# Performance work log

Measured on AMD Instinct MI355X. Metric: run time of the kernel, lower is better.

The kernel has to match this reference:

```python
import jax, jax.numpy as jnp
import numpy as np

B = 256          # graphs per batch
NN = 400         # ROI nodes per graph (N*(N-1)/2 = 79800 = input_dim)
HID = [32, 64, 128]
KS = [200, 100, 50]   # nodes kept after each TopKPooling (ratio 0.5 each)
EPS = 1e-5


def setup_inputs() -> dict:
    key = jax.random.key(0)
    ks = jax.random.split(key, 20)
    # flattened strict upper triangle of a nonnegative FC matrix per sample
    data = jax.random.uniform(ks[0], (B, NN * (NN - 1) // 2), dtype=jnp.float32)
    inp = {"data": data}
    dims = [1] + HID
    for l in range(3):
        fan_in = dims[l]
        inp[f"W{l+1}"] = jax.random.normal(ks[1 + 5 * l], (dims[l], dims[l + 1]), jnp.float32) / np.sqrt(fan_in)
        inp[f"b{l+1}"] = jnp.zeros((dims[l + 1],), jnp.float32)
        inp[f"g{l+1}"] = jnp.ones((dims[l + 1],), jnp.float32)      # BN gamma
        inp[f"be{l+1}"] = jnp.zeros((dims[l + 1],), jnp.float32)    # BN beta
        inp[f"p{l+1}"] = jax.random.normal(ks[4 + 5 * l], (dims[l + 1],), jnp.float32) * 0.1  # TopK score vector
    return inp


def _gcn_conv(A, X, W, b):
    # GCNConv with edge weights: add self loops (weight 1), symmetric D^-1/2 A D^-1/2
    n = A.shape[1]
    Al = A + jnp.eye(n, dtype=A.dtype)[None]          # (B, n, n)
    deg = Al.sum(axis=-1)                             # (B, n)
    dis = jnp.where(deg > 0, jax.lax.rsqrt(deg), 0.0)
    An = dis[:, :, None] * Al * dis[:, None, :]
    return jnp.einsum('bij,bjf->bif', An, X @ W) + b


def _block(A, X, W, b, g, be, p, k):
    # GCNConv -> ReLU -> BatchNorm(train stats) -> (dropout=identity) -> TopKPooling
    h = jax.nn.relu(_gcn_conv(A, X, W, b))
    mu = h.mean(axis=(0, 1))
    var = h.var(axis=(0, 1))
    h = (h - mu) * jax.lax.rsqrt(var + EPS) * g + be
    # TopKPooling: score = x . p / ||p||, keep top k per graph, gate by tanh(score)
    score = h @ p / jnp.linalg.norm(p)                # (B, n)
    vals, idx = jax.lax.top_k(score, k)               # (B, k)
    Xn = jnp.take_along_axis(h, idx[:, :, None], axis=1) * jnp.tanh(vals)[:, :, None]
    bi = jnp.arange(A.shape[0])[:, None, None]
    An = A[bi, idx[:, :, None], idx[:, None, :]]      # filter_adj: edges among kept nodes
    return An, Xn


def reference(data, W1, b1, g1, be1, p1, W2, b2, g2, be2, p2, W3, b3, g3, be3, p3):
    Bn = data.shape[0]
    iu0, iu1 = np.triu_indices(NN, 1)
    A = jnp.zeros((Bn, NN, NN), data.dtype).at[:, iu0, iu1].set(data)
    A = A + jnp.swapaxes(A, 1, 2)                     # symmetric FC adjacency, zero diag
    X = jnp.ones((Bn, NN, 1), data.dtype)             # initial node feature dim = 1
    A, X = _block(A, X, W1, b1, g1, be1, p1, KS[0])
    A, X = _block(A, X, W2, b2, g2, be2, p2, KS[1])
    A, X = _block(A, X, W3, b3, g3, be3, p3, KS[2])
    return X.max(axis=1)                              # global_max_pool -> (B, 128)
```

## Files before the change

kernel.cpp:

```cpp
#include <hip/hip_runtime.h>
#include <math.h>

#define BB   256
#define NN0  400
#define NE   79800
#define EPSF 1e-5f

__device__ __forceinline__ int tri_e(int a, int c) {
  return a*(NN0-1) - ((a*(a-1))>>1) + (c - a - 1);
}

__device__ __forceinline__ size_t PRI(int b, int ti, int tj, int r) {
  return (((size_t)b*7 + ti)*7 + tj)*64 + r;
}

__device__ __forceinline__ float wave_sum(float v) {
  #pragma unroll
  for (int o = 32; o > 0; o >>= 1) v += __shfl_xor(v, o, 64);
  return v;
}

__device__ __forceinline__ float rdlane(float v, int k) {
  return __int_as_float(__builtin_amdgcn_readlane(__float_as_int(v), k));
}

__device__ __forceinline__ void bitonic_desc(float* sc, int* si, int P) {
  const int tid = threadIdx.x;
  const int nt = blockDim.x;
  for (int k = 2; k <= P; k <<= 1) {
    for (int j = k >> 1; j > 0; j >>= 1) {
      __syncthreads();
      for (int i = tid; i < P; i += nt) {
        int ixj = i ^ j;
        if (ixj > i) {
          float a = sc[i], c = sc[ixj];
          int ai = si[i], ci = si[ixj];
          bool bef = (a > c) || (a == c && ai < ci);
          bool sw = ((i & k) == 0) ? !bef : bef;
          if (sw) { sc[i] = c; sc[ixj] = a; si[i] = ci; si[ixj] = ai; }
        }
      }
    }
  }
  __syncthreads();
}

__global__ __launch_bounds__(256) void k_tri_mv(
    const float* __restrict__ data,
    const float* __restrict__ pr_in, const float* __restrict__ pc_in,
    float* __restrict__ pr, float* __restrict__ pc) {
  __shared__ float tile[64][65];
  __shared__ float dI[64], dJ[64];
  const int xcd = blockIdx.x & 7, slot = blockIdx.x >> 3;
  const int b = xcd*32 + slot/7, q0 = slot % 7;
  const int tid = threadIdx.x;
  const int wave = tid >> 6, lane = tid & 63;
  const float* __restrict__ drow = data + (size_t)b*NE;
  int ti_a[4], tj_a[4];
  #pragma unroll
  for (int u = 0; u < 4; ++u) {
    int t = q0 + u*7;
    int ti = 0, rem = t;
    while (rem >= 7 - ti) { rem -= 7 - ti; ++ti; }
    ti_a[u] = ti; tj_a[u] = ti + rem;
  }
  float vreg[16];
  float rI = 0.f, rJ = 0.f;
  auto issue = [&](int u) {
    const int i0 = ti_a[u]*64, j0 = tj_a[u]*64;
    const int ni = min(64, NN0 - i0), nj = min(64, NN0 - j0);
    #pragma unroll
    for (int k = 0; k < 16; ++k) {
      const int rr = wave*16 + k;
      const int i = i0 + rr, j = j0 + lane;
      vreg[k] = 0.f;
      if (rr < ni && lane < nj && j > i) vreg[k] = drow[tri_e(i, j)];
    }
    if (pr_in) {
      if (tid < 64) {
        float a = 0.f;
        if (tid < ni) {
          const int tt = ti_a[u], r = tid;
          float acc = 1.f;
          for (int tj = tt; tj < 7; ++tj) acc += pr_in[PRI(b, tt, tj, r)];
          for (int ts = 0; ts <= tt; ++ts) acc += pc_in[PRI(b, ts, tt, r)];
          a = rsqrtf(acc);
        }
        rI = a;
      } else if (tid < 128) {
        const int c = tid - 64;
        float a = 0.f;
        if (c < nj) {
          const int tt = tj_a[u], r = c;
          float acc = 1.f;
          for (int tj = tt; tj < 7; ++tj) acc += pr_in[PRI(b, tt, tj, r)];
          for (int ts = 0; ts <= tt; ++ts) acc += pc_in[PRI(b, ts, tt, r)];
          a = rsqrtf(acc);
        }
        rJ = a;
      }
    } else {
      if (tid < 64) rI = (tid < ni) ? 1.f : 0.f;
      else if (tid < 128) rJ = (tid - 64 < nj) ? 1.f : 0.f;
    }
  };
  issue(0);
  #pragma unroll 1
  for (int u = 0; u < 4; ++u) {
    const int ti = ti_a[u], tj = tj_a[u];
    if (u) __syncthreads();
    #pragma unroll
    for (int k = 0; k < 16; ++k) tile[wave*16 + k][lane] = vreg[k];
    if (tid < 64) dI[tid] = rI;
    else if (tid < 128) dJ[tid-64] = rJ;
    __syncthreads();
    if (u + 1 < 4) issue(u + 1);
    {
      const int r = tid >> 2, q = tid & 3;
      float s = 0.f;
      #pragma unroll
      for (int c = 0; c < 16; ++c) s += tile[r][q*16 + c] * dJ[q*16 + c];
      s += __shfl_xor(s, 1, 64);
      s += __shfl_xor(s, 2, 64);
      if (q == 0) pr[PRI(b, ti, tj, r)] = s;
    }
    {
      const int c = tid >> 2, q = tid & 3;
      float s = 0.f;
      #pragma unroll
      for (int r = 0; r < 16; ++r) s += tile[q*16 + r][c] * dI[q*16 + r];
      s += __shfl_xor(s, 1, 64);
      s += __shfl_xor(s, 2, 64);
      if (q == 0) pc[PRI(b, ti, tj, c)] = s;
    }
  }
}

__global__ __launch_bounds__(256) void k_sfin_stats_red(
    const float* __restrict__ pr, const float* __restrict__ pc,
    const float* __restrict__ pr2, const float* __restrict__ pc2,
    const float* __restrict__ W1, const float* __restrict__ b1,
    float* __restrict__ s1, float* __restrict__ acc1) {
  __shared__ float sl[256];
  __shared__ float st[64];
  __shared__ float w1s[32], b1s[32];
  const int tid = threadIdx.x;
  const int i = blockIdx.x*256 + tid;
  if (tid < 32) { w1s[tid] = W1[tid]; b1s[tid] = b1[tid]; }
  if (tid < 64) st[tid] = 0.f;
  const int b = i / NN0, n = i % NN0;
  const int t = n >> 6, r = n & 63;
  float dacc = 1.f, sacc = 0.f;
  for (int tj = t; tj < 7; ++tj) { dacc += pr[PRI(b, t, tj, r)]; sacc += pr2[PRI(b, t, tj, r)]; }
  for (int ti = 0; ti <= t; ++ti) { dacc += pc[PRI(b, ti, t, r)]; sacc += pc2[PRI(b, ti, t, r)]; }
  const float d = rsqrtf(dacc);
  const float s = d * (d + sacc);
  s1[i] = s;
  sl[tid] = s;
  __syncthreads();
  const int f = tid & 31, sub = tid >> 5;
  const float w = w1s[f], bb = b1s[f];
  float S = 0.f, Q = 0.f;
  #pragma unroll
  for (int k = 0; k < 32; ++k) {
    const float ss = sl[sub*32 + k];
    const float h = fmaxf(ss*w + bb, 0.f);
    S += h; Q += h*h;
  }
  atomicAdd(&st[f], S);
  atomicAdd(&st[32+f], Q);
  __syncthreads();
  if (tid < 64) atomicAdd(&acc1[tid], st[tid]);
}

__global__ __launch_bounds__(512) void k_top1(
    const float* __restrict__ s1, const float* __restrict__ acc1,
    const float* __restrict__ W1, const float* __restrict__ b1,
    const float* __restrict__ g1, const float* __restrict__ be1,
    const float* __restrict__ p1, const float* __restrict__ W2,
    int* __restrict__ nodes2, int* __restrict__ sperm2, float* __restrict__ Y2) {
  __shared__ float sc[512]; __shared__ int si[512];
  __shared__ float sS[NN0];
  __shared__ float tvs[200];
  __shared__ int nds_l[200];
  __shared__ float w1s[32], b1s[32], cfs[32], scs[32], shs[32];
  __shared__ __align__(16) float hp[6400];
  __shared__ float c0s;
  const int tid = threadIdx.x;
  const int b = (blockIdx.x & 7)*32 + (blockIdx.x >> 3);
  if (tid < 32) { w1s[tid] = W1[tid]; b1s[tid] = b1[tid]; }
  if (tid < 64) {
    float scale = 0.f, shift = 0.f, pv = 0.f;
    if (tid < 32) {
      const float S = acc1[tid], Q = acc1[32 + tid];
      const float N = 102400.f;
      const float mu = S / N;
      const float var = Q / N - mu*mu;
      const float inv = rsqrtf(var + EPSF);
      scale = inv * g1[tid];
      shift = be1[tid] - mu * scale;
      pv = p1[tid];
    }
    const float pn = sqrtf(wave_sum(pv*pv));
    if (tid < 32) { scs[tid] = scale; shs[tid] = shift; cfs[tid] = scale*pv/pn; }
    float u = (tid < 32) ? shift*pv/pn : 0.f;
    u = wave_sum(u);
    if (tid == 0) c0s = u;
  }
  __syncthreads();
  const float c0 = c0s;
  {
    const int i = tid;
    if (i < NN0) {
      const float s = s1[(size_t)b*NN0 + i];
      sS[i] = s;
      float sco = c0;
      #pragma unroll
      for (int f = 0; f < 32; ++f) sco += fmaxf(s*w1s[f] + b1s[f], 0.f) * cfs[f];
      sc[i] = sco; si[i] = i;
    } else { sc[i] = -INFINITY; si[i] = 0x7fffffff; }
  }
  bitonic_desc(sc, si, 512);
  for (int k = tid; k < 200; k += 512) {
    tvs[k] = tanhf(sc[k]);
    nds_l[k] = si[k];
    nodes2[b*200 + k] = si[k];
  }
  __syncthreads();
  for (int o = tid; o < 6400; o += 512) {
    const int k = o >> 5, f = o & 31;
    const float s = sS[nds_l[k]];
    const float h = fmaxf(s*w1s[f] + b1s[f], 0.f);
    hp[o] = (h*scs[f] + shs[f]) * tvs[k];
  }
  __syncthreads();
  {
    const int g = tid & 63;
    float wr[32];
    #pragma unroll
    for (int f = 0; f < 32; ++f) wr[f] = W2[f*64 + g];
    for (int o = tid; o < 12800; o += 512) {
      const int k = o >> 6;
      float acc = 0.f;
      #pragma unroll
      for (int c4 = 0; c4 < 8; ++c4) {
        const float4 x4 = *(const float4*)&hp[(k<<5) + (c4<<2)];
        acc += x4.x*wr[c4*4] + x4.y*wr[c4*4+1] + x4.z*wr[c4*4+2] + x4.w*wr[c4*4+3];
      }
      Y2[(size_t)b*12800 + o] = acc;
    }
  }
  __syncthreads();
  if (tid < 256) {
    sc[tid] = (tid < 200) ? -(float)nds_l[tid] : -INFINITY;
    si[tid] = (tid < 200) ? tid : 0x7fffffff;
  }
  bitonic_desc(sc, si, 256);
  if (tid < 200) sperm2[b*200 + tid] = si[tid];
}

__global__ __launch_bounds__(256) void k_gatherA2(
    const float* __restrict__ data, const int* __restrict__ nodes2,
    const int* __restrict__ sperm2, float* __restrict__ A2, float* __restrict__ dis2) {
  __shared__ int nds[200], sp[200], sn[200];
  __shared__ float rowbuf[4][200];
  const int idx = blockIdx.x;
  const int r9 = idx >> 3;
  const int b = (idx & 7)*32 + r9/50;
  const int rg = r9 % 50;
  const int tid = threadIdx.x;
  if (tid < 200) { nds[tid] = nodes2[b*200 + tid]; sp[tid] = sperm2[b*200 + tid]; }
  __syncthreads();
  if (tid < 200) sn[tid] = nds[sp[tid]];
  __syncthreads();
  const int wave = tid >> 6, lane = tid & 63;
  const int i = rg*4 + wave;
  const int ni = nds[i];
  const float* __restrict__ drow = data + (size_t)b*NE;
  float accd = 0.f;
  for (int jj = lane; jj < 200; jj += 64) {
    const int sj = sn[jj];
    float v = 0.f;
    if (sj != ni) {
      const int a = min(ni, sj), c = max(ni, sj);
      v = drow[tri_e(a, c)];
    }
    rowbuf[wave][sp[jj]] = v;
    accd += v;
  }
  __syncthreads();
  accd = wave_sum(accd);
  const float dd = rsqrtf(1.f + accd);
  for (int j = lane; j < 200; j += 64)
    A2[((size_t)b*200 + i)*200 + j] = rowbuf[wave][j] * dd;
  if (lane == 0) dis2[b*200 + i] = dd;
}

__global__ __launch_bounds__(256) void k_conv2(
    const float* __restrict__ A2, const float* __restrict__ Y2,
    const float* __restrict__ dis2, const float* __restrict__ b2,
    float* __restrict__ h2g, float* __restrict__ acc2g) {
  __shared__ float dsb[200];
  __shared__ float st[128];
  const int tid = threadIdx.x;
  const int xcd = blockIdx.x & 7, slot = blockIdx.x >> 3;
  const int b = xcd*32 + (slot >> 3), p = slot & 7;
  const int wave = tid >> 6, lane = tid & 63;
  if (tid < 128) st[tid] = 0.f;
  if (tid < 200) dsb[tid] = dis2[b*200 + tid];
  __syncthreads();
  const float bl = b2[lane];
  const int rbl = p*25 + wave*7;
  const int lq = lane / 7, lk = lane - lq*7;
  const bool lv = (lane < 56) && (wave*7 + lk < 25);
  const float* __restrict__ Ab = A2 + (size_t)b*40000;
  const float* __restrict__ Yb = Y2 + (size_t)b*12800;
  auto ldA = [&](int j8) -> float {
    return lv ? Ab[(size_t)(j8 + lq)*200 + rbl + lk] : 0.f;
  };
  float acc[7];
  #pragma unroll
  for (int k = 0; k < 7; ++k) acc[k] = 0.f;
  float a_cur = ldA(0);
  #pragma unroll 1
  for (int jg = 0; jg < 25; ++jg) {
    const float a = a_cur;
    if (jg < 24) a_cur = ldA((jg + 1)*8);
    const int j0 = jg*8;
    #pragma unroll
    for (int q = 0; q < 8; ++q) {
      const float z = Yb[(j0 + q)*64 + lane];
      #pragma unroll
      for (int k = 0; k < 7; ++k)
        acc[k] = fmaf(rdlane(a, q*7 + k), z, acc[k]);
    }
  }
  float ss = 0.f, qq = 0.f;
  #pragma unroll
  for (int k = 0; k < 7; ++k) {
    const int lr = wave*7 + k;
    if (lr < 25) {
      const int r = p*25 + lr;
      const float d = dsb[r];
      const float y = Yb[(size_t)r*64 + lane];
      const float h = fmaxf(d*acc[k] + d*(d*y) + bl, 0.f);
      h2g[((size_t)b*200 + r)*64 + lane] = h;
      ss += h; qq += h*h;
    }
  }
  atomicAdd(&st[lane], ss);
  atomicAdd(&st[64 + lane], qq);
  __syncthreads();
  if (tid < 128) atomicAdd(&acc2g[tid], st[tid]);
}

__global__ __launch_bounds__(512) void k_top2(
    const float* __restrict__ h2g, const float* __restrict__ acc2,
    const float* __restrict__ g2, const float* __restrict__ be2,
    const float* __restrict__ p2, const float* __restrict__ W3,
    const int* __restrict__ nodes2, int* __restrict__ nodes3,
    float* __restrict__ Y3) {
  __shared__ float sc[256]; __shared__ int si[256];
  __shared__ __align__(16) float xs[6400];
  __shared__ float sc2[64], sh2[64], cf2[64];
  __shared__ float c20s;
  const int tid = threadIdx.x;
  const int b = (blockIdx.x & 7)*32 + (blockIdx.x >> 3);
  if (tid < 64) {
    const float S = acc2[tid], Q = acc2[64 + tid];
    const float N = 51200.f;
    const float mu = S/N, var = Q/N - mu*mu, inv = rsqrtf(var + EPSF);
    const float scale = inv*g2[tid], shift = be2[tid] - mu*scale;
    const float pv = p2[tid];
    const float pn = sqrtf(wave_sum(pv*pv));
    sc2[tid] = scale; sh2[tid] = shift; cf2[tid] = scale*pv/pn;
    const float u = wave_sum(shift*pv/pn);
    if (tid == 0) c20s = u;
  }
  __syncthreads();
  const int wave = tid >> 6, lane = tid & 63;
  const float cf = cf2[lane];
  const float c20 = c20s;
  for (int i = wave; i < 200; i += 8) {
    float v = h2g[((size_t)b*200 + i)*64 + lane] * cf;
    v = wave_sum(v);
    if (lane == 0) { sc[i] = v + c20; si[i] = i; }
  }
  if (tid >= 200 && tid < 256) { sc[tid] = -INFINITY; si[tid] = 0x7fffffff; }
  bitonic_desc(sc, si, 256);
  const float scale = sc2[lane], shift = sh2[lane];
  for (int o = tid; o < 6400; o += 512) {
    const int k = o >> 6;
    const int idx = si[k];
    const float tv = tanhf(sc[k]);
    xs[o] = (h2g[((size_t)b*200 + idx)*64 + lane] * scale + shift) * tv;
  }
  for (int k = tid; k < 100; k += 512) nodes3[b*100 + k] = nodes2[b*200 + si[k]];
  __syncthreads();
  {
    const int g = tid & 127;
    float wr[64];
    #pragma unroll
    for (int f = 0; f < 64; ++f) wr[f] = W3[f*128 + g];
    for (int o = tid; o < 12800; o += 512) {
      const int k = o >> 7;
      float acc = 0.f;
      #pragma unroll
      for (int c4 = 0; c4 < 16; ++c4) {
        const float4 x4 = *(const float4*)&xs[(k<<6) + (c4<<2)];
        acc += x4.x*wr[c4*4] + x4.y*wr[c4*4+1] + x4.z*wr[c4*4+2] + x4.w*wr[c4*4+3];
      }
      Y3[(size_t)b*12800 + o] = acc;
    }
  }
}

__global__ __launch_bounds__(256) void k_gatherA3(
    const float* __restrict__ data, const int* __restrict__ nodes3,
    float* __restrict__ A3, float* __restrict__ dis3) {
  __shared__ int nds[100];
  const int slot = blockIdx.x >> 3;
  const int b = (blockIdx.x & 7)*32 + slot/25, rg = slot % 25;
  const int tid = threadIdx.x;
  if (tid < 100) nds[tid] = nodes3[b*100 + tid];
  __syncthreads();
  const int wave = tid >> 6, lane = tid & 63;
  const int i = rg*4 + wave;
  const int ni = nds[i];
  const float* __restrict__ drow = data + (size_t)b*NE;
  const int j0 = lane, j1 = 64 + lane;
  float v0 = 0.f, v1 = 0.f;
  if (j0 != i) {
    const int nj = nds[j0];
    const int a = min(ni, nj), c = max(ni, nj);
    v0 = drow[tri_e(a, c)];
  }
  if (j1 < 100 && j1 != i) {
    const int nj = nds[j1];
    const int a = min(ni, nj), c = max(ni, nj);
    v1 = drow[tri_e(a, c)];
  }
  const float accd = wave_sum(v0 + v1);
  const float dd = rsqrtf(1.f + accd);
  A3[((size_t)b*100 + i)*100 + j0] = v0 * dd;
  if (j1 < 100) A3[((size_t)b*100 + i)*100 + j1] = v1 * dd;
  if (lane == 0) dis3[b*100 + i] = dd;
}

__global__ __launch_bounds__(256) void k_conv3(
    const float* __restrict__ A3, const float* __restrict__ Y3,
    const float* __restrict__ dis3, const float* __restrict__ b3,
    float* __restrict__ h3g, float* __restrict__ acc3g) {
  __shared__ float dsb[100];
  __shared__ float st[256];
  const int tid = threadIdx.x;
  const int xcd = blockIdx.x & 7, slot = blockIdx.x >> 3;
  const int b = xcd*32 + (slot >> 3), p = slot & 7;
  const int wave = tid >> 6, lane = tid & 63;
  st[tid] = 0.f;
  if (tid < 100) dsb[tid] = dis3[b*100 + tid];
  __syncthreads();
  const float bl0 = b3[lane], bl1 = b3[64 + lane];
  const int rbl = p*13 + wave*4;
  const int lq = lane >> 2, lk = lane & 3;
  const bool lvr = (wave*4 + lk < 13) && (rbl + lk < 100);
  const float* __restrict__ Ab = A3 + (size_t)b*10000;
  const float* __restrict__ Yb = Y3 + (size_t)b*12800;
  auto ldA = [&](int j16) -> float {
    return lvr ? Ab[(size_t)(j16 + lq)*100 + rbl + lk] : 0.f;
  };
  auto ldAt = [&](int j16) -> float {
    return (lvr && lq < 4) ? Ab[(size_t)(j16 + lq)*100 + rbl + lk] : 0.f;
  };
  float ac0[4], ac1[4];
  #pragma unroll
  for (int k = 0; k < 4; ++k) { ac0[k] = 0.f; ac1[k] = 0.f; }
  float a_cur = ldA(0);
  #pragma unroll 1
  for (int jg = 0; jg < 6; ++jg) {
    const float a = a_cur;
    a_cur = (jg < 5) ? ldA((jg + 1)*16) : ldAt(96);
    const int j0 = jg*16;
    #pragma unroll
    for (int q = 0; q < 16; ++q) {
      const float z0 = Yb[(j0 + q)*128 + lane];
      const float z1 = Yb[(j0 + q)*128 + 64 + lane];
      #pragma unroll
      for (int k = 0; k < 4; ++k) {
        const float av = rdlane(a, (q << 2) + k);
        ac0[k] = fmaf(av, z0, ac0[k]);
        ac1[k] = fmaf(av, z1, ac1[k]);
      }
    }
  }
  {
    const float a = a_cur;
    #pragma unroll
    for (int q = 0; q < 4; ++q) {
      const float z0 = Yb[(96 + q)*128 + lane];
      const float z1 = Yb[(96 + q)*128 + 64 + lane];
      #pragma unroll
      for (int k = 0; k < 4; ++k) {
        const float av = rdlane(a, (q << 2) + k);
        ac0[k] = fmaf(av, z0, ac0[k]);
        ac1[k] = fmaf(av, z1, ac1[k]);
      }
    }
  }
  float ss0 = 0.f, qq0 = 0.f, ss1 = 0.f, qq1 = 0.f;
  #pragma unroll
  for (int k = 0; k < 4; ++k) {
    const int lr = wave*4 + k;
    const int r = p*13 + lr;
    if (lr < 13 && r < 100) {
      const float d = dsb[r];
      const float y0 = Yb[(size_t)r*128 + lane];
      const float y1 = Yb[(size_t)r*128 + 64 + lane];
      const float h0 = fmaxf(d*ac0[k] + d*(d*y0) + bl0, 0.f);
      const float h1 = fmaxf(d*ac1[k] + d*(d*y1) + bl1, 0.f);
      h3g[((size_t)b*100 + r)*128 + lane] = h0;
      h3g[((size_t)b*100 + r)*128 + 64 + lane] = h1;
      ss0 += h0; qq0 += h0*h0; ss1 += h1; qq1 += h1*h1;
    }
  }
  atomicAdd(&st[lane], ss0);
  atomicAdd(&st[64 + lane], ss1);
  atomicAdd(&st[128 + lane], qq0);
  atomicAdd(&st[192 + lane], qq1);
  __syncthreads();
  atomicAdd(&acc3g[tid], st[tid]);
}

__global__ __launch_bounds__(256) void k_top3(
    const float* __restrict__ h3g, const float* __restrict__ acc3,
    const float* __restrict__ g3, const float* __restrict__ be3,
    const float* __restrict__ p3, float* __restrict__ out) {
  __shared__ float sc[128]; __shared__ int si[128]; __shared__ float tv[64];
  __shared__ float scl[128], shl[128], cfl[128];
  __shared__ float red2[4];
  const int tid = threadIdx.x;
  const int b = (blockIdx.x & 7)*32 + (blockIdx.x >> 3);
  const int wave = tid >> 6, lane = tid & 63;
  float scale = 0.f, shift = 0.f, pv = 0.f;
  if (tid < 128) {
    const float S = acc3[tid], Q = acc3[128 + tid];
    const float N = 25600.f;
    const float mu = S/N, var = Q/N - mu*mu, inv = rsqrtf(var + EPSF);
    scale = inv*g3[tid]; shift = be3[tid] - mu*scale; pv = p3[tid];
    const float t2 = wave_sum(pv*pv);
    if (lane == 0) red2[wave] = t2;
  }
  __syncthreads();
  const float pn = sqrtf(red2[0] + red2[1]);
  if (tid < 128) {
    scl[tid] = scale; shl[tid] = shift; cfl[tid] = scale*pv/pn;
    const float u = wave_sum(shift*pv/pn);
    if (lane == 0) red2[2 + wave] = u;
  }
  __syncthreads();
  const float c30 = red2[2] + red2[3];
  const float clo = cfl[lane], chi = cfl[64 + lane];
  for (int i = wave; i < 100; i += 4) {
    const float* hr = h3g + ((size_t)b*100 + i)*128;
    float v = hr[lane]*clo + hr[64 + lane]*chi;
    v = wave_sum(v);
    if (lane == 0) { sc[i] = v + c30; si[i] = i; }
  }
  if (tid >= 100 && tid < 128) { sc[tid] = -INFINITY; si[tid] = 0x7fffffff; }
  bitonic_desc(sc, si, 128);
  if (tid < 50) tv[tid] = tanhf(sc[tid]);
  __syncthreads();
  if (tid < 128) {
    const float scalev = scl[tid], shiftv = shl[tid];
    float m = -INFINITY;
    for (int k = 0; k < 50; ++k) {
      const float h = h3g[((size_t)b*100 + si[k])*128 + tid];
      m = fmaxf(m, (h*scalev + shiftv)*tv[k]);
    }
    out[(size_t)b*128 + tid] = m;
  }
}

extern "C" void kernel_launch(void* const* d_in, const int* in_sizes, int n_in,
                              void* d_out, int out_size, void* d_ws, size_t ws_size,
                              hipStream_t stream) {
  (void)in_sizes; (void)n_in; (void)out_size; (void)ws_size;
  const float* data = (const float*)d_in[0];
  const float* W1 = (const float*)d_in[1];
  const float* b1 = (const float*)d_in[2];
  const float* g1 = (const float*)d_in[3];
  const float* be1 = (const float*)d_in[4];
  const float* p1 = (const float*)d_in[5];
  const float* W2 = (const float*)d_in[6];
  const float* b2 = (const float*)d_in[7];
  const float* g2 = (const float*)d_in[8];
  const float* be2 = (const float*)d_in[9];
  const float* p2 = (const float*)d_in[10];
  const float* W3 = (const float*)d_in[11];
  const float* b3 = (const float*)d_in[12];
  const float* g3 = (const float*)d_in[13];
  const float* be3 = (const float*)d_in[14];
  const float* p3 = (const float*)d_in[15];
  float* out = (float*)d_out;

  char* ws = (char*)d_ws;
  size_t off = 0;
  auto alloc = [&](size_t n) { size_t o = off; off += (n + 255) & ~(size_t)255; return o; };
  float* pr     = (float*)(ws + alloc((size_t)BB*49*64*4));
  float* pc     = (float*)(ws + alloc((size_t)BB*49*64*4));
  float* pr2    = (float*)(ws + alloc((size_t)BB*49*64*4));
  float* pc2    = (float*)(ws + alloc((size_t)BB*49*64*4));
  float* s1     = (float*)(ws + alloc((size_t)BB*NN0*4));
  float* accz   = (float*)(ws + alloc(448*4));
  int*   nodes2 = (int*)  (ws + alloc((size_t)BB*200*4));
  int*   sperm2 = (int*)  (ws + alloc((size_t)BB*200*4));
  float* Y2     = (float*)(ws + alloc((size_t)BB*12800*4));
  float* A2     = (float*)(ws + alloc((size_t)BB*40000*4));
  float* dis2   = (float*)(ws + alloc((size_t)BB*200*4));
  float* h2     = (float*)(ws + alloc((size_t)BB*12800*4));
  int*   nodes3 = (int*)  (ws + alloc((size_t)BB*100*4));
  float* Y3     = (float*)(ws + alloc((size_t)BB*12800*4));
  float* A3     = (float*)(ws + alloc((size_t)BB*10000*4));
  float* dis3   = (float*)(ws + alloc((size_t)BB*100*4));
  float* h3     = (float*)(ws + alloc((size_t)BB*12800*4));
  float* acc1 = accz;
  float* acc2 = accz + 64;
  float* acc3 = accz + 192;

  hipMemsetAsync(accz, 0, 448*4, stream);
  k_tri_mv<<<dim3(BB*7), dim3(256), 0, stream>>>(data, nullptr, nullptr, pr, pc);
  k_tri_mv<<<dim3(BB*7), dim3(256), 0, stream>>>(data, pr, pc, pr2, pc2);
  k_sfin_stats_red<<<dim3(400), dim3(256), 0, stream>>>(pr, pc, pr2, pc2, W1, b1, s1, acc1);
  k_top1<<<dim3(BB), dim3(512), 0, stream>>>(s1, acc1, W1, b1, g1, be1, p1, W2, nodes2, sperm2, Y2);
  k_gatherA2<<<dim3(BB*50), dim3(256), 0, stream>>>(data, nodes2, sperm2, A2, dis2);
  k_conv2<<<dim3(BB*8), dim3(256), 0, stream>>>(A2, Y2, dis2, b2, h2, acc2);
  k_top2<<<dim3(BB), dim3(512), 0, stream>>>(h2, acc2, g2, be2, p2, W3, nodes2, nodes3, Y3);
  k_gatherA3<<<dim3(BB*25), dim3(256), 0, stream>>>(data, nodes3, A3, dis3);
  k_conv3<<<dim3(BB*8), dim3(256), 0, stream>>>(A3, Y3, dis3, b3, h3, acc3);
  k_top3<<<dim3(BB), dim3(256), 0, stream>>>(h3, acc3, g3, be3, p3, out);
}
```

Measured before the change: 453.1 us.

## Use wave-uniform scalar loads of A in GCN conv kernels instead of readlane broadcasts

The conv2 and conv3 kernels now read A entries through a wave-uniform pointer, made uniform with readfirstlane, so the compiler can emit scalar loads. This replaces the per-lane vector load followed by readlane broadcasts. Rows are also split evenly, with 5 blocks per graph and 10 or 5 rows per wave, which removes the masked-off lanes and rows, and Y loads are prefetched two rows ahead. The risk is that scalar-load latency and scalar cache bandwidth may now limit the inner loop, and the grid has fewer blocks.

```diff
diff --git a/kernel.cpp b/kernel.cpp
--- a/kernel.cpp
+++ b/kernel.cpp
@@ -20,8 +20,11 @@
   return v;
 }
 
-__device__ __forceinline__ float rdlane(float v, int k) {
-  return __int_as_float(__builtin_amdgcn_readlane(__float_as_int(v), k));
+__device__ __forceinline__ const float* lane0_ptr(const float* p) {
+  uint64_t v = (uint64_t)p;
+  uint32_t lo = (uint32_t)__builtin_amdgcn_readfirstlane((int)(v & 0xffffffffu));
+  uint32_t hi = (uint32_t)__builtin_amdgcn_readfirstlane((int)(v >> 32));
+  return (const float*)((((uint64_t)hi) << 32) | lo);
 }
 
 __device__ __forceinline__ void bitonic_desc(float* sc, int* si, int P) {
@@ -304,49 +307,40 @@
   __shared__ float st[128];
   const int tid = threadIdx.x;
   const int xcd = blockIdx.x & 7, slot = blockIdx.x >> 3;
-  const int b = xcd*32 + (slot >> 3), p = slot & 7;
+  const int b = xcd*32 + slot/5, p = slot % 5;
   const int wave = tid >> 6, lane = tid & 63;
   if (tid < 128) st[tid] = 0.f;
   if (tid < 200) dsb[tid] = dis2[b*200 + tid];
   __syncthreads();
   const float bl = b2[lane];
-  const int rbl = p*25 + wave*7;
-  const int lq = lane / 7, lk = lane - lq*7;
-  const bool lv = (lane < 56) && (wave*7 + lk < 25);
-  const float* __restrict__ Ab = A2 + (size_t)b*40000;
+  const int rb = p*40 + wave*10;
   const float* __restrict__ Yb = Y2 + (size_t)b*12800;
-  auto ldA = [&](int j8) -> float {
-    return lv ? Ab[(size_t)(j8 + lq)*200 + rbl + lk] : 0.f;
-  };
-  float acc[7];
+  const float* __restrict__ Aw = lane0_ptr(A2 + (size_t)b*40000 + rb);
+  float acc[10];
   #pragma unroll
-  for (int k = 0; k < 7; ++k) acc[k] = 0.f;
-  float a_cur = ldA(0);
-  #pragma unroll 1
-  for (int jg = 0; jg < 25; ++jg) {
-    const float a = a_cur;
-    if (jg < 24) a_cur = ldA((jg + 1)*8);
-    const int j0 = jg*8;
-    #pragma unroll
-    for (int q = 0; q < 8; ++q) {
-      const float z = Yb[(j0 + q)*64 + lane];
-      #pragma unroll
-      for (int k = 0; k < 7; ++k)
-        acc[k] = fmaf(rdlane(a, q*7 + k), z, acc[k]);
-    }
+  for (int k = 0; k < 10; ++k) acc[k] = 0.f;
+  float zA = Yb[lane], zB = Yb[64 + lane];
+  #pragma unroll 2
+  for (int jp = 0; jp < 100; ++jp) {
+    const int j = jp << 1;
+    const float za = zA, zb_ = zB;
+    if (jp < 99) { zA = Yb[(j + 2)*64 + lane]; zB = Yb[(j + 3)*64 + lane]; }
+    const float* __restrict__ Aj0 = Aw + (size_t)j*200;
+    const float* __restrict__ Aj1 = Aw + (size_t)(j + 1)*200;
+    #pragma unroll
+    for (int k = 0; k < 10; ++k) acc[k] = fmaf(Aj0[k], za, acc[k]);
+    #pragma unroll
+    for (int k = 0; k < 10; ++k) acc[k] = fmaf(Aj1[k], zb_, acc[k]);
   }
   float ss = 0.f, qq = 0.f;
   #pragma unroll
-  for (int k = 0; k < 7; ++k) {
-    const int lr = wave*7 + k;
-    if (lr < 25) {
-      const int r = p*25 + lr;
-      const float d = dsb[r];
-      const float y = Yb[(size_t)r*64 + lane];
-      const float h = fmaxf(d*acc[k] + d*(d*y) + bl, 0.f);
-      h2g[((size_t)b*200 + r)*64 + lane] = h;
-      ss += h; qq += h*h;
-    }
+  for (int k = 0; k < 10; ++k) {
+    const int r = rb + k;
+    const float d = dsb[r];
+    const float y = Yb[(size_t)r*64 + lane];
+    const float h = fmaxf(d*acc[k] + d*(d*y) + bl, 0.f);
+    h2g[((size_t)b*200 + r)*64 + lane] = h;
+    ss += h; qq += h*h;
   }
   atomicAdd(&st[lane], ss);
   atomicAdd(&st[64 + lane], qq);
@@ -455,73 +449,55 @@
   __shared__ float st[256];
   const int tid = threadIdx.x;
   const int xcd = blockIdx.x & 7, slot = blockIdx.x >> 3;
-  const int b = xcd*32 + (slot >> 3), p = slot & 7;
+  const int b = xcd*32 + slot/5, p = slot % 5;
   const int wave = tid >> 6, lane = tid & 63;
   st[tid] = 0.f;
   if (tid < 100) dsb[tid] = dis3[b*100 + tid];
   __syncthreads();
   const float bl0 = b3[lane], bl1 = b3[64 + lane];
-  const int rbl = p*13 + wave*4;
-  const int lq = lane >> 2, lk = lane & 3;
-  const bool lvr = (wave*4 + lk < 13) && (rbl + lk < 100);
-  const float* __restrict__ Ab = A3 + (size_t)b*10000;
+  const int rb = p*20 + wave*5;
   const float* __restrict__ Yb = Y3 + (size_t)b*12800;
-  auto ldA = [&](int j16) -> float {
-    return lvr ? Ab[(size_t)(j16 + lq)*100 + rbl + lk] : 0.f;
-  };
-  auto ldAt = [&](int j16) -> float {
-    return (lvr && lq < 4) ? Ab[(size_t)(j16 + lq)*100 + rbl + lk] : 0.f;
-  };
-  float ac0[4], ac1[4];
+  const float* __restrict__ Aw = lane0_ptr(A3 + (size_t)b*10000 + rb);
+  float ac0[5], ac1[5];
   #pragma unroll
-  for (int k = 0; k < 4; ++k) { ac0[k] = 0.f; ac1[k] = 0.f; }
-  float a_cur = ldA(0);
-  #pragma unroll 1
-  for (int jg = 0; jg < 6; ++jg) {
-    const float a = a_cur;
-    a_cur = (jg < 5) ? ldA((jg + 1)*16) : ldAt(96);
-    const int j0 = jg*16;
-    #pragma unroll
-    for (int q = 0; q < 16; ++q) {
-      const float z0 = Yb[(j0 + q)*128 + lane];
-      const float z1 = Yb[(j0 + q)*128 + 64 + lane];
-      #pragma unroll
-      for (int k = 0; k < 4; ++k) {
-        const float av = rdlane(a, (q << 2) + k);
-        ac0[k] = fmaf(av, z0, ac0[k]);
-        ac1[k] = fmaf(av, z1, ac1[k]);
-      }
-    }
-  }
-  {
-    const float a = a_cur;
-    #pragma unroll
-    for (int q = 0; q < 4; ++q) {
-      const float z0 = Yb[(96 + q)*128 + lane];
-      const float z1 = Yb[(96 + q)*128 + 64 + lane];
-      #pragma unroll
-      for (int k = 0; k < 4; ++k) {
-        const float av = rdlane(a, (q << 2) + k);
-        ac0[k] = fmaf(av, z0, ac0[k]);
-        ac1[k] = fmaf(av, z1, ac1[k]);
-      }
+  for (int k = 0; k < 5; ++k) { ac0[k] = 0.f; ac1[k] = 0.f; }
+  float zA0 = Yb[lane],        zA1 = Yb[64 + lane];
+  float zB0 = Yb[128 + lane],  zB1 = Yb[192 + lane];
+  #pragma unroll 2
+  for (int jp = 0; jp < 50; ++jp) {
+    const int j = jp << 1;
+    const float a0_ = zA0, a1_ = zA1, b0_ = zB0, b1_ = zB1;
+    if (jp < 49) {
+      zA0 = Yb[(j + 2)*128 + lane];  zA1 = Yb[(j + 2)*128 + 64 + lane];
+      zB0 = Yb[(j + 3)*128 + lane];  zB1 = Yb[(j + 3)*128 + 64 + lane];
+    }
+    const float* __restrict__ Aj0 = Aw + (size_t)j*100;
+    const float* __restrict__ Aj1 = Aw + (size_t)(j + 1)*100;
+    #pragma unroll
+    for (int k = 0; k < 5; ++k) {
+      const float av = Aj0[k];
+      ac0[k] = fmaf(av, a0_, ac0[k]);
+      ac1[k] = fmaf(av, a1_, ac1[k]);
+    }
+    #pragma unroll
+    for (int k = 0; k < 5; ++k) {
+      const float av = Aj1[k];
+      ac0[k] = fmaf(av, b0_, ac0[k]);
+      ac1[k] = fmaf(av, b1_, ac1[k]);
     }
   }
   float ss0 = 0.f, qq0 = 0.f, ss1 = 0.f, qq1 = 0.f;
   #pragma unroll
-  for (int k = 0; k < 4; ++k) {
-    const int lr = wave*4 + k;
-    const int r = p*13 + lr;
-    if (lr < 13 && r < 100) {
-      const float d = dsb[r];
-      const float y0 = Yb[(size_t)r*128 + lane];
-      const float y1 = Yb[(size_t)r*128 + 64 + lane];
-      const float h0 = fmaxf(d*ac0[k] + d*(d*y0) + bl0, 0.f);
-      const float h1 = fmaxf(d*ac1[k] + d*(d*y1) + bl1, 0.f);
-      h3g[((size_t)b*100 + r)*128 + lane] = h0;
-      h3g[((size_t)b*100 + r)*128 + 64 + lane] = h1;
-      ss0 += h0; qq0 += h0*h0; ss1 += h1; qq1 += h1*h1;
-    }
+  for (int k = 0; k < 5; ++k) {
+    const int r = rb + k;
+    const float d = dsb[r];
+    const float y0 = Yb[(size_t)r*128 + lane];
+    const float y1 = Yb[(size_t)r*128 + 64 + lane];
+    const float h0 = fmaxf(d*ac0[k] + d*(d*y0) + bl0, 0.f);
+    const float h1 = fmaxf(d*ac1[k] + d*(d*y1) + bl1, 0.f);
+    h3g[((size_t)b*100 + r)*128 + lane] = h0;
+    h3g[((size_t)b*100 + r)*128 + 64 + lane] = h1;
+    ss0 += h0; qq0 += h0*h0; ss1 += h1; qq1 += h1*h1;
   }
   atomicAdd(&st[lane], ss0);
   atomicAdd(&st[64 + lane], ss1);
@@ -633,9 +609,9 @@
   k_sfin_stats_red<<<dim3(400), dim3(256), 0, stream>>>(pr, pc, pr2, pc2, W1, b1, s1, acc1);
   k_top1<<<dim3(BB), dim3(512), 0, stream>>>(s1, acc1, W1, b1, g1, be1, p1, W2, nodes2, sperm2, Y2);
   k_gatherA2<<<dim3(BB*50), dim3(256), 0, stream>>>(data, nodes2, sperm2, A2, dis2);
-  k_conv2<<<dim3(BB*8), dim3(256), 0, stream>>>(A2, Y2, dis2, b2, h2, acc2);
+  k_conv2<<<dim3(BB*5), dim3(256), 0, stream>>>(A2, Y2, dis2, b2, h2, acc2);
   k_top2<<<dim3(BB), dim3(512), 0, stream>>>(h2, acc2, g2, be2, p2, W3, nodes2, nodes3, Y3);
   k_gatherA3<<<dim3(BB*25), dim3(256), 0, stream>>>(data, nodes3, A3, dis3);
-  k_conv3<<<dim3(BB*8), dim3(256), 0, stream>>>(A3, Y3, dis3, b3, h3, acc3);
+  k_conv3<<<dim3(BB*5), dim3(256), 0, stream>>>(A3, Y3, dis3, b3, h3, acc3);
   k_top3<<<dim3(BB), dim3(256), 0, stream>>>(h3, acc3, g3, be3, p3, out);
 }
```

Result: slower. 496.2 us (+9.5%).
